# Optimization experiments

Measured on AMD Instinct MI355X. Metric: run time of the kernel, lower is better.

## Reference

```python
import jax, jax.numpy as jnp
import numpy as np

B, P, N, D = 32, 100, 1000, 128
SQRT_D = 11.313708498984761
CLIP = 10.0


def setup_inputs() -> dict:
    key = jax.random.key(0)
    ks = jax.random.split(key, 8)
    s = 1.0 / np.sqrt(D)  # keep k ~ N(0,1) so exp(k) is stable
    return {
        "encoded_nodes": jax.random.normal(ks[0], (B, N, D), jnp.float32),
        "encoded_q1": jax.random.normal(ks[1], (B, P, D), jnp.float32),
        "encoded_last_node": jax.random.normal(ks[2], (B, P, D), jnp.float32),
        "cur_dist": jax.random.uniform(ks[3], (B, P, N), jnp.float32),
        "ninf_mask": jnp.zeros((B, P, N), jnp.float32),
        "log_scale": jnp.ones((1,), jnp.float32),
        "Wq_first": jax.random.normal(ks[4], (D, D), jnp.float32) * s,
        "Wq_last": jax.random.normal(ks[5], (D, D), jnp.float32) * s,
        "Wk": jax.random.normal(ks[6], (D, D), jnp.float32) * s,
        "Wv": jax.random.normal(ks[7], (D, D), jnp.float32) * s,
        "dist_alpha_1": jnp.ones((1,), jnp.float32),
        "AFT_dist_alpha_1": jnp.ones((1,), jnp.float32),
    }


def reference(encoded_nodes, encoded_q1, encoded_last_node, cur_dist, ninf_mask,
              log_scale, Wq_first, Wq_last, Wk, Wv, dist_alpha_1, AFT_dist_alpha_1):
    # set_kv / set_q1 (torch Linear: x @ W.T)
    k = jnp.einsum('bnd,ed->bne', encoded_nodes, Wk)          # [B,N,D]
    v = jnp.einsum('bnd,ed->bne', encoded_nodes, Wv)          # [B,N,D]
    q_first = jnp.einsum('bpd,ed->bpe', encoded_q1, Wq_first) # [B,P,D]
    q_last = jnp.einsum('bpd,ed->bpe', encoded_last_node, Wq_last)
    q = q_first + q_last

    cur_dist_out = -cur_dist                                   # [B,P,N]
    bias_scale = log_scale * AFT_dist_alpha_1 * cur_dist_out + ninf_mask
    ebias = jnp.exp(bias_scale)                                # [B,P,N]
    ek = jnp.exp(k)                                            # [B,N,D]
    num = jnp.einsum('bpn,bnd->bpd', ebias, ek * v)
    den = jnp.einsum('bpn,bnd->bpd', ebias, ek)
    aft_out = jax.nn.sigmoid(q) * (num / den)                  # [B,P,D]

    score = jnp.einsum('bpd,bnd->bpn', aft_out, encoded_nodes) / SQRT_D
    score = score + log_scale * dist_alpha_1 * cur_dist_out
    score = CLIP * jnp.tanh(score) + ninf_mask
    return jax.nn.softmax(score, axis=2)
```

## Files before the change

kernel.cpp:

```cpp
#include <hip/hip_runtime.h>
#include <hip/hip_bf16.h>
#include <math.h>

#define B 32
#define P 100
#define N 1000
#define D 128

constexpr float SQRT_D_INV = 1.0f / 11.313708498984761f;
constexpr float CLIPV = 10.0f;

__device__ __forceinline__ void fma4(float4& a, float s, const float4& b) {
    a.x = fmaf(s, b.x, a.x);
    a.y = fmaf(s, b.y, a.y);
    a.z = fmaf(s, b.z, a.z);
    a.w = fmaf(s, b.w, a.w);
}

#define TT 64
__global__ __launch_bounds__(256) void prep_kernel(
        const float* __restrict__ nodes,
        const float* __restrict__ Wk,  const float* __restrict__ Wv,
        const float* __restrict__ Wqf, const float* __restrict__ Wql,
        float* __restrict__ wkT,  float* __restrict__ wvT,
        float* __restrict__ wqfT, float* __restrict__ wqlT,
        float* __restrict__ nodesT) {
    const int t = threadIdx.x;
    if (blockIdx.x < D) {
        const int e = blockIdx.x;
        const int d = t & 127;
        if ((t >> 7) == 0) {
            wkT[e * D + d] = Wk[d * D + e];
            wvT[e * D + d] = Wv[d * D + e];
        } else {
            wqfT[e * D + d] = Wqf[d * D + e];
            wqlT[e * D + d] = Wql[d * D + e];
        }
        return;
    }
    __shared__ float sh[TT][D + 1];
    const int blk = blockIdx.x - D;
    const int ntiles = (N + TT - 1) / TT;
    const int b  = blk / ntiles;
    const int n0 = (blk % ntiles) * TT;
    const int rows = min(TT, N - n0);

    const float4* src = (const float4*)(nodes + ((long)b * N + n0) * D);
    for (int i = t; i < rows * (D / 4); i += 256) {
        int r = i >> 5, c = i & 31;
        float4 v = src[(long)r * (D / 4) + c];
        sh[r][c * 4 + 0] = v.x; sh[r][c * 4 + 1] = v.y;
        sh[r][c * 4 + 2] = v.z; sh[r][c * 4 + 3] = v.w;
    }
    __syncthreads();

    const int nl = t & 63;
    const int eg = t >> 6;
    if (nl < rows) {
        #pragma unroll
        for (int k = 0; k < 32; ++k) {
            int e = eg * 32 + k;
            nodesT[((long)b * D + e) * N + n0 + nl] = sh[nl][e];
        }
    }
}

#define R1 32
__global__ __launch_bounds__(256) void kv_kernel(
        const float* __restrict__ nodes,
        const float* __restrict__ wkT,
        const float* __restrict__ wvT,
        float* __restrict__ ek,
        float* __restrict__ ekv) {
    __shared__ float sh[R1][D];
    const int t = threadIdx.x;
    const int dq = t & 31;
    const int rl = t >> 5;
    const long row0 = (long)blockIdx.x * R1;

    const float4* src = (const float4*)(nodes + row0 * D);
    float4* dst = (float4*)(&sh[0][0]);
    #pragma unroll
    for (int i = 0; i < (R1 * D / 4) / 256; ++i)
        dst[t + i * 256] = src[t + i * 256];
    __syncthreads();

    float4 ka[4], va[4];
    #pragma unroll
    for (int rr = 0; rr < 4; ++rr) {
        ka[rr] = make_float4(0.f, 0.f, 0.f, 0.f);
        va[rr] = make_float4(0.f, 0.f, 0.f, 0.f);
    }

    const float* wkp = wkT + dq * 4;
    const float* wvp = wvT + dq * 4;

    float4 cwk[4], cwv[4];
    #pragma unroll
    for (int ee = 0; ee < 4; ++ee) {
        cwk[ee] = *(const float4*)(wkp + ee * D);
        cwv[ee] = *(const float4*)(wvp + ee * D);
    }

    for (int e0 = 0; e0 < D; e0 += 4) {
        float4 nwk[4], nwv[4];
        if (e0 + 4 < D) {
            #pragma unroll
            for (int ee = 0; ee < 4; ++ee) {
                nwk[ee] = *(const float4*)(wkp + (e0 + 4 + ee) * D);
                nwv[ee] = *(const float4*)(wvp + (e0 + 4 + ee) * D);
            }
        }
        #pragma unroll
        for (int rr = 0; rr < 4; ++rr) {
            float4 s4 = *(const float4*)(&sh[rl * 4 + rr][e0]);
            fma4(ka[rr], s4.x, cwk[0]); fma4(ka[rr], s4.y, cwk[1]);
            fma4(ka[rr], s4.z, cwk[2]); fma4(ka[rr], s4.w, cwk[3]);
            fma4(va[rr], s4.x, cwv[0]); fma4(va[rr], s4.y, cwv[1]);
            fma4(va[rr], s4.z, cwv[2]); fma4(va[rr], s4.w, cwv[3]);
        }
        #pragma unroll
        for (int ee = 0; ee < 4; ++ee) { cwk[ee] = nwk[ee]; cwv[ee] = nwv[ee]; }
    }

    #pragma unroll
    for (int rr = 0; rr < 4; ++rr) {
        long row = row0 + rl * 4 + rr;
        float4 e4;
        e4.x = __expf(ka[rr].x); e4.y = __expf(ka[rr].y);
        e4.z = __expf(ka[rr].z); e4.w = __expf(ka[rr].w);
        float4 ev;
        ev.x = e4.x * va[rr].x; ev.y = e4.y * va[rr].y;
        ev.z = e4.z * va[rr].z; ev.w = e4.w * va[rr].w;
        *(float4*)(ek + row * D + dq * 4) = e4;
        *(float4*)(ekv + row * D + dq * 4) = ev;
    }
}

#define R2 16
__global__ __launch_bounds__(256) void q_kernel(
        const float* __restrict__ q1,
        const float* __restrict__ qlast,
        const float* __restrict__ wqfT,
        const float* __restrict__ wqlT,
        float* __restrict__ qsig) {
    __shared__ float sh1[R2][D];
    __shared__ float sh2[R2][D];
    const int t = threadIdx.x;
    const int dq = t & 31;
    const int rl = t >> 5;
    const long row0 = (long)blockIdx.x * R2;

    const float4* s1 = (const float4*)(q1 + row0 * D);
    const float4* s2 = (const float4*)(qlast + row0 * D);
    float4* d1 = (float4*)(&sh1[0][0]);
    float4* d2 = (float4*)(&sh2[0][0]);
    #pragma unroll
    for (int i = 0; i < (R2 * D / 4) / 256; ++i) {
        d1[t + i * 256] = s1[t + i * 256];
        d2[t + i * 256] = s2[t + i * 256];
    }
    __syncthreads();

    float4 acc[2];
    acc[0] = make_float4(0.f, 0.f, 0.f, 0.f);
    acc[1] = make_float4(0.f, 0.f, 0.f, 0.f);

    const float* wfp = wqfT + dq * 4;
    const float* wlp = wqlT + dq * 4;

    float4 cwf[4], cwl[4];
    #pragma unroll
    for (int ee = 0; ee < 4; ++ee) {
        cwf[ee] = *(const float4*)(wfp + ee * D);
        cwl[ee] = *(const float4*)(wlp + ee * D);
    }

    for (int e0 = 0; e0 < D; e0 += 4) {
        float4 nwf[4], nwl[4];
        if (e0 + 4 < D) {
            #pragma unroll
            for (int ee = 0; ee < 4; ++ee) {
                nwf[ee] = *(const float4*)(wfp + (e0 + 4 + ee) * D);
                nwl[ee] = *(const float4*)(wlp + (e0 + 4 + ee) * D);
            }
        }
        #pragma unroll
        for (int rr = 0; rr < 2; ++rr) {
            float4 a4 = *(const float4*)(&sh1[rl * 2 + rr][e0]);
            float4 b4 = *(const float4*)(&sh2[rl * 2 + rr][e0]);
            fma4(acc[rr], a4.x, cwf[0]); fma4(acc[rr], a4.y, cwf[1]);
            fma4(acc[rr], a4.z, cwf[2]); fma4(acc[rr], a4.w, cwf[3]);
            fma4(acc[rr], b4.x, cwl[0]); fma4(acc[rr], b4.y, cwl[1]);
            fma4(acc[rr], b4.z, cwl[2]); fma4(acc[rr], b4.w, cwl[3]);
        }
        #pragma unroll
        for (int ee = 0; ee < 4; ++ee) { cwf[ee] = nwf[ee]; cwl[ee] = nwl[ee]; }
    }

    #pragma unroll
    for (int rr = 0; rr < 2; ++rr) {
        long row = row0 + rl * 2 + rr;
        float4 s;
        s.x = 1.0f / (1.0f + __expf(-acc[rr].x));
        s.y = 1.0f / (1.0f + __expf(-acc[rr].y));
        s.z = 1.0f / (1.0f + __expf(-acc[rr].z));
        s.w = 1.0f / (1.0f + __expf(-acc[rr].w));
        *(float4*)(qsig + row * D + dq * 4) = s;
    }
}

#define PT 20
#define TS 32
__global__ __launch_bounds__(128) void aft_part_kernel(
        const float* __restrict__ cur_dist,
        const float* __restrict__ ninf,
        const float* __restrict__ ek,
        const float* __restrict__ ekv,
        const float* __restrict__ log_scale,
        const float* __restrict__ aft_alpha,
        float* __restrict__ pnum,
        float* __restrict__ pden,
        int NC, int L) {
    __shared__ float eb[2][TS][33];
    const int t = threadIdx.x;
    const int dq = t & 31;
    const int pl = t >> 5;
    const int pl5 = pl * 5;
    const int c  = blockIdx.x % NC;
    const int pt = (blockIdx.x / NC) % (P / PT);
    const int b  = blockIdx.x / (NC * (P / PT));
    const int p0 = pt * PT;
    const int n_begin = c * L;
    const int n_end = min(N, n_begin + L);
    const float lsA = log_scale[0] * aft_alpha[0];

    float4 num[5], den[5];
    #pragma unroll
    for (int i = 0; i < 5; ++i) {
        num[i] = make_float4(0.f, 0.f, 0.f, 0.f);
        den[i] = make_float4(0.f, 0.f, 0.f, 0.f);
    }

    float rv[5];
    int n0 = n_begin;
    int ts = min(TS, n_end - n0);

    #pragma unroll
    for (int k = 0; k < 5; ++k) {
        int s = t + k * 128;
        int pp = s >> 5, nl = s & 31;
        rv[k] = 0.f;
        if (nl < ts) {
            long idx = ((long)b * P + p0 + pp) * N + (n0 + nl);
            rv[k] = fmaf(-lsA, cur_dist[idx], ninf[idx]);
        }
    }

    int buf = 0;
    while (n0 < n_end) {
        #pragma unroll
        for (int k = 0; k < 5; ++k) {
            int s = t + k * 128;
            int pp = s >> 5, nl = s & 31;
            if (nl < ts) eb[buf][nl][pp] = __expf(rv[k]);
        }
        __syncthreads();

        const int n0n = n0 + ts;
        const int tsn = min(TS, n_end - n0n);
        if (n0n < n_end) {
            #pragma unroll
            for (int k = 0; k < 5; ++k) {
                int s = t + k * 128;
                int pp = s >> 5, nl = s & 31;
                rv[k] = 0.f;
                if (nl < tsn) {
                    long idx = ((long)b * P + p0 + pp) * N + (n0n + nl);
                    rv[k] = fmaf(-lsA, cur_dist[idx], ninf[idx]);
                }
            }
        }

        const float* ekb = ek  + ((long)b * N + n0) * D + dq * 4;
        const float* evb = ekv + ((long)b * N + n0) * D + dq * 4;
        #pragma unroll 4
        for (int j = 0; j < ts; ++j) {
            float4 ekq = *(const float4*)(ekb + (long)j * D);
            float4 evq = *(const float4*)(evb + (long)j * D);
            float e0 = eb[buf][j][pl5 + 0];
            float e1 = eb[buf][j][pl5 + 1];
            float e2 = eb[buf][j][pl5 + 2];
            float e3 = eb[buf][j][pl5 + 3];
            float e4 = eb[buf][j][pl5 + 4];
            fma4(num[0], e0, evq); fma4(den[0], e0, ekq);
            fma4(num[1], e1, evq); fma4(den[1], e1, ekq);
            fma4(num[2], e2, evq); fma4(den[2], e2, ekq);
            fma4(num[3], e3, evq); fma4(den[3], e3, ekq);
            fma4(num[4], e4, evq); fma4(den[4], e4, ekq);
        }
        buf ^= 1;
        n0 = n0n;
        ts = tsn;
    }

    #pragma unroll
    for (int r = 0; r < 5; ++r) {
        int p = p0 + pl5 + r;
        long o = (((long)c * B + b) * P + p) * D + dq * 4;
        *(float4*)(pnum + o) = num[r];
        *(float4*)(pden + o) = den[r];
    }
}

#define PT2 10
__global__ __launch_bounds__(512) void score_kernel(
        const float* __restrict__ pnum,
        const float* __restrict__ pden,
        const float* __restrict__ qsig,
        const float* __restrict__ nodesT,
        const float* __restrict__ cur_dist,
        const float* __restrict__ ninf,
        const float* __restrict__ log_scale,
        const float* __restrict__ dist_alpha,
        float* __restrict__ out, int NC) {
    __shared__ float sa[PT2][D];
    __shared__ float red[8][PT2];
    __shared__ float bmax[PT2];
    __shared__ float bsum[PT2];
    const int t = threadIdx.x;
    const int wid = t >> 6;
    const int pt = blockIdx.x % (P / PT2);
    const int b  = blockIdx.x / (P / PT2);
    const int p0 = pt * PT2;
    const float lsA = log_scale[0] * dist_alpha[0];
    const long BPD = (long)B * P * D;

    for (int idx = t; idx < PT2 * D; idx += 512) {
        int i = idx >> 7;
        int d = idx & 127;
        long o = ((long)b * P + p0 + i) * D + d;
        float nsum = 0.f, dsum = 0.f;
        for (int c = 0; c < NC; ++c) {
            nsum += pnum[(long)c * BPD + o];
            dsum += pden[(long)c * BPD + o];
        }
        sa[i][d] = qsig[o] * nsum / dsum;
    }
    __syncthreads();

    const int n0 = t * 2;
    const bool act = (n0 < N);
    const int ncl = act ? n0 : 0;
    const float* ntb = nodesT + (long)b * D * N;

    float2 acc[PT2];
    #pragma unroll
    for (int i = 0; i < PT2; ++i) acc[i] = make_float2(0.f, 0.f);

    float2 cx[4];
    #pragma unroll
    for (int ee = 0; ee < 4; ++ee)
        cx[ee] = *(const float2*)(ntb + (long)ee * N + ncl);

    for (int e0 = 0; e0 < D; e0 += 4) {
        float2 nx[4];
        if (e0 + 4 < D) {
            #pragma unroll
            for (int ee = 0; ee < 4; ++ee)
                nx[ee] = *(const float2*)(ntb + (long)(e0 + 4 + ee) * N + ncl);
        }
        #pragma unroll
        for (int i = 0; i < PT2; ++i) {
            float4 a4 = *(const float4*)(&sa[i][e0]);
            acc[i].x = fmaf(cx[0].x, a4.x, acc[i].x);
            acc[i].x = fmaf(cx[1].x, a4.y, acc[i].x);
            acc[i].x = fmaf(cx[2].x, a4.z, acc[i].x);
            acc[i].x = fmaf(cx[3].x, a4.w, acc[i].x);
            acc[i].y = fmaf(cx[0].y, a4.x, acc[i].y);
            acc[i].y = fmaf(cx[1].y, a4.y, acc[i].y);
            acc[i].y = fmaf(cx[2].y, a4.z, acc[i].y);
            acc[i].y = fmaf(cx[3].y, a4.w, acc[i].y);
        }
        #pragma unroll
        for (int ee = 0; ee < 4; ++ee) cx[ee] = nx[ee];
    }

    float2 sc[PT2];
    #pragma unroll
    for (int i = 0; i < PT2; ++i) {
        if (act) {
            long idx = ((long)b * P + p0 + i) * N + n0;
            float2 cd = *(const float2*)(cur_dist + idx);
            float2 nf = *(const float2*)(ninf + idx);
            float sx = fmaf(acc[i].x, SQRT_D_INV, -lsA * cd.x);
            float sy = fmaf(acc[i].y, SQRT_D_INV, -lsA * cd.y);
            float ax = fabsf(sx), ay = fabsf(sy);
            float rx = 1.f - 2.f / (__expf(2.f * ax) + 1.f);
            float ry = 1.f - 2.f / (__expf(2.f * ay) + 1.f);
            sc[i].x = CLIPV * copysignf(rx, sx) + nf.x;
            sc[i].y = CLIPV * copysignf(ry, sy) + nf.y;
        } else {
            sc[i].x = -INFINITY;
            sc[i].y = -INFINITY;
        }
    }

    #pragma unroll
    for (int i = 0; i < PT2; ++i) {
        float m = fmaxf(sc[i].x, sc[i].y);
        #pragma unroll
        for (int o = 1; o < 64; o <<= 1) m = fmaxf(m, __shfl_xor(m, o, 64));
        if ((t & 63) == 0) red[wid][i] = m;
    }
    __syncthreads();
    if (t < PT2) {
        float mm = red[0][t];
        #pragma unroll
        for (int w = 1; w < 8; ++w) mm = fmaxf(mm, red[w][t]);
        bmax[t] = mm;
    }
    __syncthreads();

    float2 ex[PT2];
    #pragma unroll
    for (int i = 0; i < PT2; ++i) {
        float m = bmax[i];
        ex[i].x = (sc[i].x > -1e30f) ? __expf(sc[i].x - m) : 0.f;
        ex[i].y = (sc[i].y > -1e30f) ? __expf(sc[i].y - m) : 0.f;
        float ssum = ex[i].x + ex[i].y;
        #pragma unroll
        for (int o = 1; o < 64; o <<= 1) ssum += __shfl_xor(ssum, o, 64);
        if ((t & 63) == 0) red[wid][i] = ssum;
    }
    __syncthreads();
    if (t < PT2) {
        float ss = red[0][t];
        #pragma unroll
        for (int w = 1; w < 8; ++w) ss += red[w][t];
        bsum[t] = ss;
    }
    __syncthreads();

    #pragma unroll
    for (int i = 0; i < PT2; ++i) {
        if (act) {
            float inv = 1.0f / bsum[i];
            long idx = ((long)b * P + p0 + i) * N + n0;
            *(float2*)(out + idx) = make_float2(ex[i].x * inv, ex[i].y * inv);
        }
    }
}

extern "C" void kernel_launch(void* const* d_in, const int* in_sizes, int n_in,
                              void* d_out, int out_size, void* d_ws, size_t ws_size,
                              hipStream_t stream) {
    const float* nodes      = (const float*)d_in[0];
    const float* q1         = (const float*)d_in[1];
    const float* qlast      = (const float*)d_in[2];
    const float* cur_dist   = (const float*)d_in[3];
    const float* ninf       = (const float*)d_in[4];
    const float* log_scale  = (const float*)d_in[5];
    const float* Wqf        = (const float*)d_in[6];
    const float* Wql        = (const float*)d_in[7];
    const float* Wk         = (const float*)d_in[8];
    const float* Wv         = (const float*)d_in[9];
    const float* dist_alpha = (const float*)d_in[10];
    const float* aft_alpha  = (const float*)d_in[11];
    float* out = (float*)d_out;

    const long BND = (long)B * N * D;
    const long BPD = (long)B * P * D;
    const long W2  = (long)D * D;

    float* ws     = (float*)d_ws;
    float* ek     = ws;
    float* ekv    = ek + BND;
    float* qsig   = ekv + BND;
    float* wkT    = qsig + BPD;
    float* wvT    = wkT + W2;
    float* wqfT   = wvT + W2;
    float* wqlT   = wqfT + W2;
    float* nodesT = wqlT + W2;
    float* pnum   = nodesT + BND;

    long avail = (long)(ws_size / 4) - (3 * BND + BPD + 4 * W2);
    int NC = (int)(avail / (2 * BPD));
    if (NC < 1) NC = 1;
    if (NC > 12) NC = 12;
    int L = (N + NC - 1) / NC;
    NC = (N + L - 1) / L;
    float* pden = pnum + (long)NC * BPD;

    prep_kernel<<<D + B * ((N + TT - 1) / TT), 256, 0, stream>>>(
        nodes, Wk, Wv, Wqf, Wql, wkT, wvT, wqfT, wqlT, nodesT);
    kv_kernel<<<(B * N) / R1, 256, 0, stream>>>(nodes, wkT, wvT, ek, ekv);
    q_kernel<<<(B * P) / R2, 256, 0, stream>>>(q1, qlast, wqfT, wqlT, qsig);
    aft_part_kernel<<<B * (P / PT) * NC, 128, 0, stream>>>(
        cur_dist, ninf, ek, ekv, log_scale, aft_alpha, pnum, pden, NC, L);
    score_kernel<<<B * (P / PT2), 512, 0, stream>>>(
        pnum, pden, qsig, nodesT, cur_dist, ninf, log_scale, dist_alpha, out, NC);
}
```

Before: 250.2 us.

## Split score kernel across N chunks with atomic softmax sums and separate normalize

The per-block partial reduction of num/den moves into its own elementwise kernel. The score kernel is split into four N-chunks per (b, p-tile) with 128 threads, and it drops the max subtraction because tanh clipping bounds scores to ±10. Each block writes unnormalized exp values and atomically adds row sums, then a normalize kernel rescales each row. Block index ordering is also changed so that b varies fastest for better L2 locality. The change raises parallelism in the score stage at the cost of two extra launches, a memset, and an extra read/write pass over the output.

Result: no change. 247.6 us (-1.0%).

```diff
diff --git a/kernel.cpp b/kernel.cpp
--- a/kernel.cpp
+++ b/kernel.cpp
@@ -227,9 +227,10 @@
     const int dq = t & 31;
     const int pl = t >> 5;
     const int pl5 = pl * 5;
-    const int c  = blockIdx.x % NC;
-    const int pt = (blockIdx.x / NC) % (P / PT);
-    const int b  = blockIdx.x / (NC * (P / PT));
+    const int b    = blockIdx.x % B;
+    const int rest = blockIdx.x / B;
+    const int c    = rest % NC;
+    const int pt   = rest / NC;
     const int p0 = pt * PT;
     const int n_begin = c * L;
     const int n_end = min(N, n_begin + L);
@@ -313,43 +314,50 @@
     }
 }
 
-#define PT2 10
-__global__ __launch_bounds__(512) void score_kernel(
+__global__ __launch_bounds__(256) void aft_reduce_kernel(
         const float* __restrict__ pnum,
         const float* __restrict__ pden,
         const float* __restrict__ qsig,
+        float* __restrict__ aft,
+        int NC) {
+    const long i = (long)blockIdx.x * 256 + threadIdx.x;
+    const long BPD = (long)B * P * D;
+    float n = 0.f, d = 0.f;
+    for (int c = 0; c < NC; ++c) {
+        n += pnum[(long)c * BPD + i];
+        d += pden[(long)c * BPD + i];
+    }
+    aft[i] = qsig[i] * n / d;
+}
+
+#define PT2 10
+#define SC 4
+__global__ __launch_bounds__(128) void score_part_kernel(
+        const float* __restrict__ aft,
         const float* __restrict__ nodesT,
         const float* __restrict__ cur_dist,
         const float* __restrict__ ninf,
         const float* __restrict__ log_scale,
         const float* __restrict__ dist_alpha,
-        float* __restrict__ out, int NC) {
+        float* __restrict__ out,
+        float* __restrict__ sums) {
     __shared__ float sa[PT2][D];
-    __shared__ float red[8][PT2];
-    __shared__ float bmax[PT2];
-    __shared__ float bsum[PT2];
+    __shared__ float red[2][PT2];
     const int t = threadIdx.x;
     const int wid = t >> 6;
-    const int pt = blockIdx.x % (P / PT2);
-    const int b  = blockIdx.x / (P / PT2);
+    const int b    = blockIdx.x % B;
+    const int rest = blockIdx.x / B;
+    const int c    = rest % SC;
+    const int pt   = rest / SC;
     const int p0 = pt * PT2;
     const float lsA = log_scale[0] * dist_alpha[0];
-    const long BPD = (long)B * P * D;
-
-    for (int idx = t; idx < PT2 * D; idx += 512) {
-        int i = idx >> 7;
-        int d = idx & 127;
-        long o = ((long)b * P + p0 + i) * D + d;
-        float nsum = 0.f, dsum = 0.f;
-        for (int c = 0; c < NC; ++c) {
-            nsum += pnum[(long)c * BPD + o];
-            dsum += pden[(long)c * BPD + o];
-        }
-        sa[i][d] = qsig[o] * nsum / dsum;
+
+    for (int i = t; i < PT2 * D; i += 128) {
+        sa[i >> 7][i & 127] = aft[((long)b * P + p0) * D + i];
     }
     __syncthreads();
 
-    const int n0 = t * 2;
+    const int n0 = c * 256 + t * 2;
     const bool act = (n0 < N);
     const int ncl = act ? n0 : 0;
     const float* ntb = nodesT + (long)b * D * N;
@@ -386,9 +394,9 @@
         for (int ee = 0; ee < 4; ++ee) cx[ee] = nx[ee];
     }
 
-    float2 sc[PT2];
     #pragma unroll
     for (int i = 0; i < PT2; ++i) {
+        float2 ev = make_float2(0.f, 0.f);
         if (act) {
             long idx = ((long)b * P + p0 + i) * N + n0;
             float2 cd = *(const float2*)(cur_dist + idx);
@@ -398,57 +406,33 @@
             float ax = fabsf(sx), ay = fabsf(sy);
             float rx = 1.f - 2.f / (__expf(2.f * ax) + 1.f);
             float ry = 1.f - 2.f / (__expf(2.f * ay) + 1.f);
-            sc[i].x = CLIPV * copysignf(rx, sx) + nf.x;
-            sc[i].y = CLIPV * copysignf(ry, sy) + nf.y;
-        } else {
-            sc[i].x = -INFINITY;
-            sc[i].y = -INFINITY;
-        }
-    }
-
-    #pragma unroll
-    for (int i = 0; i < PT2; ++i) {
-        float m = fmaxf(sc[i].x, sc[i].y);
-        #pragma unroll
-        for (int o = 1; o < 64; o <<= 1) m = fmaxf(m, __shfl_xor(m, o, 64));
-        if ((t & 63) == 0) red[wid][i] = m;
+            float scx = CLIPV * copysignf(rx, sx) + nf.x;
+            float scy = CLIPV * copysignf(ry, sy) + nf.y;
+            ev.x = __expf(scx);
+            ev.y = __expf(scy);
+            *(float2*)(out + idx) = ev;
+        }
+        float s = ev.x + ev.y;
+        #pragma unroll
+        for (int o = 1; o < 64; o <<= 1) s += __shfl_xor(s, o, 64);
+        if ((t & 63) == 0) red[wid][i] = s;
     }
     __syncthreads();
     if (t < PT2) {
-        float mm = red[0][t];
-        #pragma unroll
-        for (int w = 1; w < 8; ++w) mm = fmaxf(mm, red[w][t]);
-        bmax[t] = mm;
-    }
-    __syncthreads();
-
-    float2 ex[PT2];
-    #pragma unroll
-    for (int i = 0; i < PT2; ++i) {
-        float m = bmax[i];
-        ex[i].x = (sc[i].x > -1e30f) ? __expf(sc[i].x - m) : 0.f;
-        ex[i].y = (sc[i].y > -1e30f) ? __expf(sc[i].y - m) : 0.f;
-        float ssum = ex[i].x + ex[i].y;
-        #pragma unroll
-        for (int o = 1; o < 64; o <<= 1) ssum += __shfl_xor(ssum, o, 64);
-        if ((t & 63) == 0) red[wid][i] = ssum;
-    }
-    __syncthreads();
-    if (t < PT2) {
-        float ss = red[0][t];
-        #pragma unroll
-        for (int w = 1; w < 8; ++w) ss += red[w][t];
-        bsum[t] = ss;
-    }
-    __syncthreads();
-
-    #pragma unroll
-    for (int i = 0; i < PT2; ++i) {
-        if (act) {
-            float inv = 1.0f / bsum[i];
-            long idx = ((long)b * P + p0 + i) * N + n0;
-            *(float2*)(out + idx) = make_float2(ex[i].x * inv, ex[i].y * inv);
-        }
+        atomicAdd(&sums[b * P + p0 + t], red[0][t] + red[1][t]);
+    }
+}
+
+__global__ __launch_bounds__(256) void normalize_kernel(
+        float* __restrict__ out, const float* __restrict__ sums) {
+    const int row = blockIdx.x;
+    const int t = threadIdx.x;
+    const float inv = 1.0f / sums[row];
+    float4* r = (float4*)(out + (long)row * N);
+    if (t < N / 4) {
+        float4 v = r[t];
+        v.x *= inv; v.y *= inv; v.z *= inv; v.w *= inv;
+        r[t] = v;
     }
 }
 
@@ -477,14 +461,16 @@
     float* ek     = ws;
     float* ekv    = ek + BND;
     float* qsig   = ekv + BND;
-    float* wkT    = qsig + BPD;
+    float* aft    = qsig + BPD;
+    float* wkT    = aft + BPD;
     float* wvT    = wkT + W2;
     float* wqfT   = wvT + W2;
     float* wqlT   = wqfT + W2;
     float* nodesT = wqlT + W2;
-    float* pnum   = nodesT + BND;
-
-    long avail = (long)(ws_size / 4) - (3 * BND + BPD + 4 * W2);
+    float* sums   = nodesT + BND;
+    float* pnum   = sums + (long)B * P;
+
+    long avail = (long)(ws_size / 4) - (3 * BND + 2 * BPD + 4 * W2 + (long)B * P);
     int NC = (int)(avail / (2 * BPD));
     if (NC < 1) NC = 1;
     if (NC > 12) NC = 12;
@@ -492,12 +478,15 @@
     NC = (N + L - 1) / L;
     float* pden = pnum + (long)NC * BPD;
 
+    hipMemsetAsync(sums, 0, (size_t)B * P * sizeof(float), stream);
     prep_kernel<<<D + B * ((N + TT - 1) / TT), 256, 0, stream>>>(
         nodes, Wk, Wv, Wqf, Wql, wkT, wvT, wqfT, wqlT, nodesT);
     kv_kernel<<<(B * N) / R1, 256, 0, stream>>>(nodes, wkT, wvT, ek, ekv);
     q_kernel<<<(B * P) / R2, 256, 0, stream>>>(q1, qlast, wqfT, wqlT, qsig);
     aft_part_kernel<<<B * (P / PT) * NC, 128, 0, stream>>>(
         cur_dist, ninf, ek, ekv, log_scale, aft_alpha, pnum, pden, NC, L);
-    score_kernel<<<B * (P / PT2), 512, 0, stream>>>(
-        pnum, pden, qsig, nodesT, cur_dist, ninf, log_scale, dist_alpha, out, NC);
-}
+    aft_reduce_kernel<<<(int)(BPD / 256), 256, 0, stream>>>(pnum, pden, qsig, aft, NC);
+    score_part_kernel<<<B * SC * (P / PT2), 128, 0, stream>>>(
+        aft, nodesT, cur_dist, ninf, log_scale, dist_alpha, out, sums);
+    normalize_kernel<<<B * P, 256, 0, stream>>>(out, sums);
+}
```
